# Kernel optimization log

Measured on AMD Instinct MI355X. Metric: run time of the kernel, lower is better.

The kernel has to match this reference:

```python
import jax, jax.numpy as jnp
import numpy as np
import math

H = 8        # num_heads
D = 1024     # per-head dim (d_q = d_k = d_v)
D_I = 1024   # image embed dim
D_L = 768    # sentence embed dim
EPS = 1e-5   # nn.LayerNorm default


def setup_inputs() -> dict:
    key = jax.random.key(0)
    ks = jax.random.split(key, 8)
    B, NQ, NK = 8, 196, 128
    img_embed = jax.random.normal(ks[0], (B, NQ, D_I), dtype=jnp.float32)
    sent_embed = jax.random.normal(ks[1], (B, NK, D_L), dtype=jnp.float32)
    atten_mask = jnp.ones((B, NK), dtype=jnp.int32)
    # weights stored [in, out] (equivalent to torch Linear weight.T), no bias
    Wq = jax.random.normal(ks[2], (D_I, H * D), dtype=jnp.float32) * (1.0 / math.sqrt(D_I))
    Wk = jax.random.normal(ks[3], (D_L, H * D), dtype=jnp.float32) * (1.0 / math.sqrt(D_L))
    Wv = jax.random.normal(ks[4], (D_L, H * D), dtype=jnp.float32) * (1.0 / math.sqrt(D_L))
    Wo = jax.random.normal(ks[5], (H * D, D_I), dtype=jnp.float32) * (1.0 / math.sqrt(H * D))
    gamma = jnp.ones((D_I,), dtype=jnp.float32)
    beta = jnp.zeros((D_I,), dtype=jnp.float32)
    return {"img_embed": img_embed, "sent_embed": sent_embed, "atten_mask": atten_mask,
            "Wq": Wq, "Wk": Wk, "Wv": Wv, "Wo": Wo, "gamma": gamma, "beta": beta}


def reference(img_embed, sent_embed, atten_mask, Wq, Wk, Wv, Wo, gamma, beta):
    B = img_embed.shape[0]
    # projections -> [B, N, H, D] -> [B, H, N, D]
    Q = (img_embed @ Wq).reshape(B, -1, H, D).transpose(0, 2, 1, 3)
    K = (sent_embed @ Wk).reshape(B, -1, H, D).transpose(0, 2, 1, 3)
    V = (sent_embed @ Wv).reshape(B, -1, H, D).transpose(0, 2, 1, 3)
    # scaled dot-product scores [B, H, NQ, NK]
    score = jnp.einsum('bhqd,bhkd->bhqk', Q, K) / math.sqrt(D)
    mask = (atten_mask != 0)[:, None, None, :]  # [B,1,1,NK]
    score = jnp.where(mask, score, -jnp.inf)
    attn = jax.nn.softmax(score, axis=-1)
    # PV -> [B, NQ, H, D] -> [B, NQ, H*D]
    ctx = jnp.einsum('bhqk,bhkd->bqhd', attn, V).reshape(B, -1, H * D)
    out = ctx @ Wo + img_embed  # residual
    # LayerNorm over last dim
    mu = jnp.mean(out, axis=-1, keepdims=True)
    var = jnp.var(out, axis=-1, keepdims=True)
    return (out - mu) * jax.lax.rsqrt(var + EPS) * gamma + beta
```

## Files before the change

### kernel.cpp

```cpp
#include <hip/hip_runtime.h>
#include <hip/hip_bf16.h>

#define BB 8
#define NQ 196
#define NKK 128
#define HH 8
#define DH 1024
#define DI 1024
#define DL 768
#define HD 8192
#define KSPLIT 8

typedef __attribute__((ext_vector_type(8))) short short8;
typedef __attribute__((ext_vector_type(4))) float f32x4;

__device__ inline unsigned short f2bf(float f) {
  unsigned int x = __float_as_uint(f);
  unsigned int r = (x + 0x7fffu + ((x >> 16) & 1u)) >> 16;
  return (unsigned short)r;
}

__device__ inline void gload16(const unsigned short* g, unsigned short* l) {
  __builtin_amdgcn_global_load_lds(
      (const __attribute__((address_space(1))) void*)g,
      (__attribute__((address_space(3))) void*)l, 16, 0, 0);
}

__global__ __launch_bounds__(256) void k_prep(
    const float* __restrict__ Wq, const float* __restrict__ Wk,
    const float* __restrict__ Wv, const float* __restrict__ Wo,
    const float* __restrict__ img, const float* __restrict__ sent,
    unsigned short* __restrict__ WqT, unsigned short* __restrict__ WkvT,
    unsigned short* __restrict__ WoT,
    unsigned short* __restrict__ imgB, unsigned short* __restrict__ sentB) {
  int b = blockIdx.x, t = threadIdx.x;
  if (b >= 7168) {
    const float* in; unsigned short* out; int i;
    if (b < 7952) { in = img;  out = imgB;  i = ((b - 7168) * 256 + t) * 8; }
    else          { in = sent; out = sentB; i = ((b - 7952) * 256 + t) * 8; }
    float4 x = *reinterpret_cast<const float4*>(in + i);
    float4 y = *reinterpret_cast<const float4*>(in + i + 4);
    short8 v;
    v[0] = (short)f2bf(x.x); v[1] = (short)f2bf(x.y);
    v[2] = (short)f2bf(x.z); v[3] = (short)f2bf(x.w);
    v[4] = (short)f2bf(y.x); v[5] = (short)f2bf(y.y);
    v[6] = (short)f2bf(y.z); v[7] = (short)f2bf(y.w);
    *reinterpret_cast<short8*>(out + i) = v;
    return;
  }
  const float* in; unsigned short* out; int R, C, bx;
  if (b < 2048)      { in = Wq; out = WqT;  R = DI; C = HD; bx = b; }
  else if (b < 3584) { in = Wk; out = WkvT; R = DL; C = HD; bx = b - 2048; }
  else if (b < 5120) { in = Wv; out = WkvT + (size_t)HD * DL; R = DL; C = HD; bx = b - 3584; }
  else               { in = Wo; out = WoT;  R = HD; C = DI; bx = b - 5120; }
  int nxc = C >> 6;
  int c0 = (bx % nxc) << 6, r0 = (bx / nxc) << 6;
  __shared__ float tile[64][65];
#pragma unroll
  for (int p = 0; p < 4; ++p) {
    int row = p * 16 + (t >> 4), c4 = (t & 15) << 2;
    float4 v = *reinterpret_cast<const float4*>(&in[(size_t)(r0 + row) * C + c0 + c4]);
    tile[row][c4] = v.x; tile[row][c4 + 1] = v.y;
    tile[row][c4 + 2] = v.z; tile[row][c4 + 3] = v.w;
  }
  __syncthreads();
#pragma unroll
  for (int p = 0; p < 2; ++p) {
    int cc = p * 32 + (t >> 3), r8 = (t & 7) << 3;
    short8 w;
#pragma unroll
    for (int j = 0; j < 8; ++j) w[j] = (short)f2bf(tile[r8 + j][cc]);
    *reinterpret_cast<short8*>(&out[(size_t)(c0 + cc) * R + r0 + r8]) = w;
  }
}

__global__ __launch_bounds__(256) void k_transpose_v(
    const unsigned short* __restrict__ Vp, unsigned short* __restrict__ Vt, int ld_in) {
  __shared__ unsigned short tile[32][34];
  int z = blockIdx.z, b = z >> 3, h = z & 7;
  const unsigned short* in = Vp + (size_t)b * NKK * ld_in + (size_t)h * DH;
  unsigned short* out = Vt + (size_t)z * DH * NKK;
  int d0 = blockIdx.x * 32, k0 = blockIdx.y * 32;
  {
    int rr = threadIdx.x >> 3, c4 = (threadIdx.x & 7) << 2;
    ushort4 v = *reinterpret_cast<const ushort4*>(&in[(size_t)(k0 + rr) * ld_in + d0 + c4]);
    tile[rr][c4] = v.x; tile[rr][c4 + 1] = v.y;
    tile[rr][c4 + 2] = v.z; tile[rr][c4 + 3] = v.w;
  }
  __syncthreads();
  {
    int cc = threadIdx.x >> 3, r4 = (threadIdx.x & 7) << 2;
    ushort4 w;
    w.x = tile[r4][cc];     w.y = tile[r4 + 1][cc];
    w.z = tile[r4 + 2][cc]; w.w = tile[r4 + 3][cc];
    *reinterpret_cast<ushort4*>(&out[(size_t)(d0 + cc) * NKK + k0 + r4]) = w;
  }
}


__device__ __attribute__((always_inline)) inline void ph_pre() {
  __builtin_amdgcn_s_barrier();
  asm volatile("s_waitcnt lgkmcnt(0)" ::: "memory");
  __builtin_amdgcn_sched_barrier(0);
  __builtin_amdgcn_s_setprio(1);
}
__device__ __attribute__((always_inline)) inline void ph_post() {
  __builtin_amdgcn_s_setprio(0);
  __builtin_amdgcn_s_barrier();
}
__device__ __attribute__((always_inline)) inline void ph_post_vm4() {
  __builtin_amdgcn_s_setprio(0);
  asm volatile("s_waitcnt vmcnt(4)" ::: "memory");
  __builtin_amdgcn_s_barrier();
}
__device__ __attribute__((always_inline)) inline void ph_post_vm0() {
  __builtin_amdgcn_s_setprio(0);
  asm volatile("s_waitcnt vmcnt(0)" ::: "memory");
  __builtin_amdgcn_s_barrier();
}

#define LDA8(d, buf, s)                                                          \
  { _Pragma("unroll") for (int mi = 0; mi < 4; ++mi) {                           \
      const int row_ = wm * 128 + (s) * 64 + mi * 16 + fr;                       \
      d[mi][0] = *reinterpret_cast<const short8*>(&As[buf][row_ * 64 + swz0]);   \
      d[mi][1] = *reinterpret_cast<const short8*>(&As[buf][row_ * 64 + swz1]);   \
    } }
#define LDB8(d, buf, s)                                                          \
  { _Pragma("unroll") for (int ni = 0; ni < 2; ++ni) {                           \
      const int row_ = wn * 64 + (s) * 32 + ni * 16 + fr;                        \
      d[ni][0] = *reinterpret_cast<const short8*>(&Bs[buf][row_ * 64 + swz0]);   \
      d[ni][1] = *reinterpret_cast<const short8*>(&Bs[buf][row_ * 64 + swz1]);   \
    } }
#define MMQ(a, sa, b, sb)                                                        \
  { _Pragma("unroll") for (int kk = 0; kk < 2; ++kk) {                           \
      _Pragma("unroll") for (int mi = 0; mi < 4; ++mi) {                         \
        _Pragma("unroll") for (int ni = 0; ni < 2; ++ni)                         \
          acc[(sa) * 4 + mi][(sb) * 2 + ni] =                                    \
              __builtin_amdgcn_mfma_f32_16x16x32_bf16(                           \
                  a[mi][kk], b[ni][kk], acc[(sa) * 4 + mi][(sb) * 2 + ni], 0, 0, 0); \
      } } }
#define STA8(buf, h, kof)                                                        \
  { gload16(aS[h][0] + (kof), &As[buf][(h) * 8192 + wid * 512]);                 \
    gload16(aS[h][1] + (kof), &As[buf][(h) * 8192 + 4096 + wid * 512]); }
#define STB8(buf, h, kof)                                                        \
  { gload16(bS[h][0] + (kof), &Bs[buf][(h) * 8192 + wid * 512]);                 \
    gload16(bS[h][1] + (kof), &Bs[buf][(h) * 8192 + 4096 + wid * 512]); }

struct GCfg {
  const unsigned short* A; const unsigned short* B; void* C;
  int M, K, lda, ldb, ldc, nx, ny;
  long aKC, bKC, cKC;
};

template<bool C_BF16>
__global__ __launch_bounds__(512, 2) void k_gemm8(GCfg c0, GCfg c1, int split) {
  __shared__ unsigned short As[2][16384];
  __shared__ unsigned short Bs[2][16384];

  const int seg = (int)blockIdx.x >= split;
  const GCfg cfg = seg ? c1 : c0;
  const int o = (int)blockIdx.x - (seg ? split : 0);
  const int nseg = seg ? ((int)gridDim.x - split) : split;
  const int qq = nseg >> 3;
  const int g = (o & 7) * qq + (o >> 3);
  const int ybl = g % cfg.ny; int t1 = g / cfg.ny;
  const int xbl = t1 % cfg.nx; const int kc = t1 / cfg.nx;

  const int M = cfg.M, lda = cfg.lda, ldb = cfg.ldb;
  const unsigned short* Ab = cfg.A + (size_t)kc * cfg.aKC;
  const unsigned short* Bb = cfg.B + (size_t)kc * cfg.bKC;

  const int tid = threadIdx.x, lane = tid & 63, wid = tid >> 6;
  const int wm = wid >> 2, wn = wid & 3;
  const int m_base = ybl * 256, n_base = xbl * 256;
  const int fr = lane & 15, qk = lane >> 4;
  const int swz0 = ((qk ^ (fr & 7)) << 3);
  const int swz1 = (((4 + qk) ^ (fr & 7)) << 3);

  const int srow = lane >> 3;
  const int sc8 = (((lane & 7) ^ srow) << 3);
  const unsigned short* aS[2][2];
  const unsigned short* bS[2][2];
#pragma unroll
  for (int h = 0; h < 2; ++h)
#pragma unroll
    for (int j = 0; j < 2; ++j) {
      int rm = m_base + h * 128 + j * 64 + wid * 8 + srow;
      rm = rm < M ? rm : M - 1;
      aS[h][j] = Ab + (size_t)rm * lda + sc8;
      bS[h][j] = Bb + (size_t)(n_base + h * 128 + j * 64 + wid * 8 + srow) * ldb + sc8;
    }

  short8 a0[4][2], a1[4][2], b0[2][2], b1[2][2];
  f32x4 acc[8][4] = {};

  const int NT = cfg.K >> 6;
  const int NIT = NT >> 1;

  STB8(0, 0, 0) STB8(0, 1, 0) STA8(0, 0, 0) STA8(0, 1, 0)
  STB8(1, 0, 64) STB8(1, 1, 64)
  asm volatile("s_waitcnt vmcnt(4)" ::: "memory");
  __builtin_amdgcn_s_barrier();

  for (int it = 0; it < NIT - 1; ++it) {
    const int t1k = (2 * it + 1) << 6;
    const int t2k = (2 * it + 2) << 6;
    const int t3k = (2 * it + 3) << 6;
    LDA8(a0, 0, 0) LDB8(b0, 0, 0) STA8(1, 0, t1k)
    ph_pre(); MMQ(a0, 0, b0, 0) ph_post();
    LDB8(b1, 0, 1) STA8(1, 1, t1k)
    ph_pre(); MMQ(a0, 0, b1, 1) ph_post();
    LDA8(a1, 0, 1) STB8(0, 0, t2k)
    ph_pre(); MMQ(a1, 1, b1, 1) ph_post();
    STB8(0, 1, t2k)
    ph_pre(); MMQ(a1, 1, b0, 0) ph_post_vm4();
    LDA8(a0, 1, 0) LDB8(b0, 1, 0) STA8(0, 0, t2k)
    ph_pre(); MMQ(a0, 0, b0, 0) ph_post();
    LDB8(b1, 1, 1) STA8(0, 1, t2k)
    ph_pre(); MMQ(a0, 0, b1, 1) ph_post();
    LDA8(a1, 1, 1) STB8(1, 0, t3k)
    ph_pre(); MMQ(a1, 1, b1, 1) ph_post();
    STB8(1, 1, t3k)
    ph_pre(); MMQ(a1, 1, b0, 0) ph_post_vm4();
  }

  {
    const int tlk = (NT - 1) << 6;
    LDA8(a0, 0, 0) LDB8(b0, 0, 0) STA8(1, 0, tlk)
    ph_pre(); MMQ(a0, 0, b0, 0) ph_post();
    LDB8(b1, 0, 1) STA8(1, 1, tlk)
    ph_pre(); MMQ(a0, 0, b1, 1) ph_post();
    LDA8(a1, 0, 1)
    ph_pre(); MMQ(a1, 1, b1, 1) ph_post();
    ph_pre(); MMQ(a1, 1, b0, 0) ph_post_vm0();
    LDA8(a0, 1, 0) LDB8(b0, 1, 0)
    ph_pre(); MMQ(a0, 0, b0, 0) ph_post();
    LDB8(b1, 1, 1)
    ph_pre(); MMQ(a0, 0, b1, 1) ph_post();
    LDA8(a1, 1, 1)
    ph_pre(); MMQ(a1, 1, b1, 1) ph_post();
    ph_pre(); MMQ(a1, 1, b0, 0)
    __builtin_amdgcn_s_setprio(0);
  }

  const size_t cOff = (size_t)kc * cfg.cKC;
  const int ldc = cfg.ldc;
  const int rq4 = qk * 4;
#pragma unroll
  for (int mi = 0; mi < 8; ++mi) {
#pragma unroll
    for (int ni = 0; ni < 4; ++ni) {
      int col = n_base + wn * 64 + ni * 16 + fr;
#pragma unroll
      for (int i = 0; i < 4; ++i) {
        int row = m_base + wm * 128 + mi * 16 + rq4 + i;
        if (row < M) {
          float val = acc[mi][ni][i];
          size_t off = cOff + (size_t)row * ldc + col;
          if constexpr (C_BF16) ((unsigned short*)cfg.C)[off] = f2bf(val);
          else                  ((float*)cfg.C)[off] = val;
        }
      }
    }
  }
}

template<bool C_BF16>
__global__ __launch_bounds__(256, 2) void k_gemm3(
    const unsigned short* __restrict__ A, const unsigned short* __restrict__ B,
    void* __restrict__ Cptr,
    int M, int K, int lda, int ldb, int ldc,
    int nx, int ny, int ZBH,
    long aSB, long aSH, long bSB, long bSH, long cSB, long cSH,
    long aKC, long bKC, long cKC) {
  __shared__ unsigned short As[8192];
  __shared__ unsigned short Bs[8192];

  const int nblk = gridDim.x;
  const int qq = nblk >> 3, rr = nblk & 7;
  int g;
  { const int o = blockIdx.x, xcd = o & 7, i = o >> 3;
    g = (xcd < rr ? xcd * (qq + 1) : rr * (qq + 1) + (xcd - rr) * qq) + i; }
  const int ybl = g % ny; int t1 = g / ny;
  const int xbl = t1 % nx; const int zz = t1 / nx;
  const int kc = zz / ZBH, bh = zz % ZBH;
  const int zb = bh >> 3, zh = bh & 7;

  const unsigned short* Ab = A + (size_t)zb * aSB + (size_t)zh * aSH + (size_t)kc * aKC;
  const unsigned short* Bb = B + (size_t)zb * bSB + (size_t)zh * bSH + (size_t)kc * bKC;

  const int tid = threadIdx.x, lane = tid & 63, wid = tid >> 6;
  const int wm = wid >> 1, wn = wid & 1;
  const int m_base = ybl * 128, n_base = xbl * 128;

  const int r0 = wid * 32 + (lane >> 3);
  const int sc8 = (((lane & 7) ^ (lane >> 3)) << 3);
  const unsigned short* aSrc[4];
  const unsigned short* bSrc[4];
#pragma unroll
  for (int p = 0; p < 4; ++p) {
    int rm = m_base + r0 + p * 8; rm = rm < M ? rm : M - 1;
    aSrc[p] = Ab + (size_t)rm * lda + sc8;
    bSrc[p] = Bb + (size_t)(n_base + r0 + p * 8) * ldb + sc8;
  }

  const int fr = lane & 15;
  const int qk = lane >> 4;
  f32x4 acc[4][4] = {};

  for (int k0 = 0; k0 < K; k0 += 64) {
#pragma unroll
    for (int p = 0; p < 4; ++p) gload16(aSrc[p] + k0, &As[wid * 2048 + p * 512]);
#pragma unroll
    for (int p = 0; p < 4; ++p) gload16(bSrc[p] + k0, &Bs[wid * 2048 + p * 512]);
    __syncthreads();
#pragma unroll
    for (int kk = 0; kk < 2; ++kk) {
      short8 af[4], bfr[4];
#pragma unroll
      for (int mi = 0; mi < 4; ++mi) {
        int row = wm * 64 + mi * 16 + fr;
        int swz = ((kk * 4 + qk) ^ (row & 7)) << 3;
        af[mi] = *reinterpret_cast<const short8*>(&As[row * 64 + swz]);
      }
#pragma unroll
      for (int ni = 0; ni < 4; ++ni) {
        int row = wn * 64 + ni * 16 + fr;
        int swz = ((kk * 4 + qk) ^ (row & 7)) << 3;
        bfr[ni] = *reinterpret_cast<const short8*>(&Bs[row * 64 + swz]);
      }
#pragma unroll
      for (int mi = 0; mi < 4; ++mi)
#pragma unroll
        for (int ni = 0; ni < 4; ++ni)
          acc[mi][ni] = __builtin_amdgcn_mfma_f32_16x16x32_bf16(af[mi], bfr[ni], acc[mi][ni], 0, 0, 0);
    }
    __syncthreads();
  }

  const size_t cOff = (size_t)zb * cSB + (size_t)zh * cSH + (size_t)kc * cKC;
  const int rq = qk * 4;
#pragma unroll
  for (int mi = 0; mi < 4; ++mi) {
#pragma unroll
    for (int ni = 0; ni < 4; ++ni) {
      int col = n_base + wn * 64 + ni * 16 + fr;
#pragma unroll
      for (int i = 0; i < 4; ++i) {
        int row = m_base + wm * 64 + mi * 16 + rq + i;
        if (row < M) {
          float val = acc[mi][ni][i];
          size_t off = cOff + (size_t)row * ldc + col;
          if constexpr (C_BF16) ((unsigned short*)Cptr)[off] = f2bf(val);
          else                  ((float*)Cptr)[off] = val;
        }
      }
    }
  }
}

#define S_PART ((size_t)64 * NQ * NKK)
__global__ __launch_bounds__(256) void k_softmax(
    const float* __restrict__ S, unsigned short* __restrict__ P, const int* __restrict__ mask) {
  int row = blockIdx.x * 4 + (threadIdx.x >> 6);
  if (row >= BB * HH * NQ) return;
  int lane = threadIdx.x & 63;
  int b = row / (HH * NQ);
  const float* s = S + (size_t)row * NKK;
  float s0 = (s[lane]      + s[lane + S_PART])      * 0.03125f;
  float s1 = (s[lane + 64] + s[lane + 64 + S_PART]) * 0.03125f;
  const int* mrow = mask + b * NKK;
  if (mrow[lane] == 0)      s0 = -1e30f;
  if (mrow[lane + 64] == 0) s1 = -1e30f;
  float mx = fmaxf(s0, s1);
#pragma unroll
  for (int d = 32; d; d >>= 1) mx = fmaxf(mx, __shfl_xor(mx, d));
  float e0 = __expf(s0 - mx), e1 = __expf(s1 - mx);
  float sum = e0 + e1;
#pragma unroll
  for (int d = 32; d; d >>= 1) sum += __shfl_xor(sum, d);
  float inv = 1.0f / sum;
  P[(size_t)row * NKK + lane]      = f2bf(e0 * inv);
  P[(size_t)row * NKK + lane + 64] = f2bf(e1 * inv);
}

__global__ __launch_bounds__(256) void k_layernorm_red(
    const float* __restrict__ Parts, const float* __restrict__ resid,
    const float* __restrict__ gamma, const float* __restrict__ beta,
    float* __restrict__ out, int M) {
  int row = blockIdx.x;
  int tid = threadIdx.x;
  const size_t stride = (size_t)M * DI;
  const float* p = Parts + (size_t)row * DI;
  const float* r = resid + (size_t)row * DI;
  float v[4], sum = 0.f, sq = 0.f;
#pragma unroll
  for (int i = 0; i < 4; ++i) {
    int c = tid + i * 256;
    float acc = r[c];
#pragma unroll
    for (int k = 0; k < KSPLIT; ++k) acc += p[k * stride + c];
    v[i] = acc; sum += acc; sq += acc * acc;
  }
#pragma unroll
  for (int d = 32; d; d >>= 1) { sum += __shfl_xor(sum, d); sq += __shfl_xor(sq, d); }
  __shared__ float ssum[4], ssq[4];
  int w = tid >> 6;
  if ((tid & 63) == 0) { ssum[w] = sum; ssq[w] = sq; }
  __syncthreads();
  sum = ssum[0] + ssum[1] + ssum[2] + ssum[3];
  sq  = ssq[0]  + ssq[1]  + ssq[2]  + ssq[3];
  float mean = sum * (1.0f / DI);
  float var  = sq * (1.0f / DI) - mean * mean;
  float rstd = rsqrtf(var + 1e-5f);
  float* o = out + (size_t)row * DI;
#pragma unroll
  for (int i = 0; i < 4; ++i) {
    int c = tid + i * 256;
    o[c] = (v[i] - mean) * rstd * gamma[c] + beta[c];
  }
}

extern "C" void kernel_launch(void* const* d_in, const int* in_sizes, int n_in,
                              void* d_out, int out_size, void* d_ws, size_t ws_size,
                              hipStream_t stream) {
  const float* img   = (const float*)d_in[0];
  const float* sent  = (const float*)d_in[1];
  const int*   mask  = (const int*)d_in[2];
  const float* Wq    = (const float*)d_in[3];
  const float* Wk    = (const float*)d_in[4];
  const float* Wv    = (const float*)d_in[5];
  const float* Wo    = (const float*)d_in[6];
  const float* gamma = (const float*)d_in[7];
  const float* beta  = (const float*)d_in[8];
  float* out = (float*)d_out;

  char* ws = (char*)d_ws;
  unsigned short* WoT   = (unsigned short*)(ws);
  unsigned short* WkvT  = (unsigned short*)(ws + 16777216);
  unsigned short* Vt    = (unsigned short*)(ws + 16777216);
  float*          Oac   = (float*)         (ws + 16777216);
  float*          S2    = (float*)         (ws + 33554432);
  unsigned short* P     = (unsigned short*)(ws + 46399488);
  unsigned short* Qb    = (unsigned short*)(ws + 49610752);
  unsigned short* KVb   = (unsigned short*)(ws + 75300864);
  unsigned short* ctx   = (unsigned short*)(ws + 75300864);
  unsigned short* WqT   = (unsigned short*)(ws + 75300864);
  unsigned short* imgB  = (unsigned short*)(ws + 92078080);
  unsigned short* sentB = (unsigned short*)(ws + 108855296);

  dim3 tb(256);
  dim3 tb8(512);

  k_prep<<<dim3(8336), tb, 0, stream>>>(Wq, Wk, Wv, Wo, img, sent,
                                        WqT, WkvT, WoT, imgB, sentB);

  GCfg cfgQ  = { imgB,  WqT,  Qb,  BB * NQ,  DI, DI, DI, HD,      32, 7, 0, 0, 0 };
  GCfg cfgKV = { sentB, WkvT, KVb, BB * NKK, DL, DL, DL, 2 * HD,  64, 4, 0, 0, 0 };
  k_gemm8<true><<<dim3(224 + 256), tb8, 0, stream>>>(cfgQ, cfgKV, 224);

  k_transpose_v<<<dim3(DH / 32, NKK / 32, BB * HH), tb, 0, stream>>>(KVb + HD, Vt, 2 * HD);

  k_gemm3<false><<<dim3(2 * 1 * 128), tb, 0, stream>>>(
      Qb, KVb, S2, NQ, DH / 2, HD, 2 * HD, NKK,
      1, 2, 64,
      (long)NQ * HD, (long)DH, (long)NKK * 2 * HD, (long)DH,
      (long)HH * NQ * NKK, (long)NQ * NKK,
      (long)(DH / 2), (long)(DH / 2), (long)64 * NQ * NKK);

  k_softmax<<<dim3(BB * HH * NQ / 4), tb, 0, stream>>>(S2, P, mask);

  k_gemm3<true><<<dim3(2 * 8 * 64), tb, 0, stream>>>(
      P, Vt, ctx, NQ, NKK, NKK, NKK, HD,
      8, 2, 64,
      (long)HH * NQ * NKK, (long)NQ * NKK, (long)HH * DH * NKK, (long)DH * NKK,
      (long)NQ * HD, (long)DH, 0, 0, 0);

  GCfg cfgO = { ctx, WoT, Oac, BB * NQ, HD / KSPLIT, HD, HD, DI, 4, 7,
                (long)(HD / KSPLIT), (long)(HD / KSPLIT), (long)(BB * NQ) * DI };
  k_gemm8<false><<<dim3(224), tb8, 0, stream>>>(cfgO, cfgO, 224);

  k_layernorm_red<<<dim3(BB * NQ), tb, 0, stream>>>(Oac, img, gamma, beta, out, BB * NQ);
}
```

Before: 187.5 us.

## Store Q/K/V, context and Wo in head-blocked 1024-wide chunks

The projection GEMM epilogue now writes Q, K and V head-blocked, each head's 1024 columns stored as a contiguous chunk with row stride 1024 instead of interleaved rows of 8192 or 16384. The Wo transpose, the V transpose, the attention GEMMs and the output GEMM are re-strided to match. Per-head and per-K-split tiles therefore become dense 2 KB-stride regions, which is meant to improve locality and reduce TLB and cache-set pressure. It adds some index arithmetic in the epilogues, and every stride in the chain has to stay consistent.

Result: no change. 187.1 us (-0.2%).

```diff
diff --git a/kernel.cpp b/kernel.cpp
--- a/kernel.cpp
+++ b/kernel.cpp
@@ -10,6 +10,9 @@
 #define DL 768
 #define HD 8192
 #define KSPLIT 8
+#define MTOT (BB * NQ)
+#define CHK (MTOT * DH)
+#define KVCHK (1024 * 1024)
 
 typedef __attribute__((ext_vector_type(8))) short short8;
 typedef __attribute__((ext_vector_type(4))) float f32x4;
@@ -48,11 +51,11 @@
     *reinterpret_cast<short8*>(out + i) = v;
     return;
   }
-  const float* in; unsigned short* out; int R, C, bx;
+  const float* in; unsigned short* out; int R, C, bx; bool kcb = false;
   if (b < 2048)      { in = Wq; out = WqT;  R = DI; C = HD; bx = b; }
   else if (b < 3584) { in = Wk; out = WkvT; R = DL; C = HD; bx = b - 2048; }
   else if (b < 5120) { in = Wv; out = WkvT + (size_t)HD * DL; R = DL; C = HD; bx = b - 3584; }
-  else               { in = Wo; out = WoT;  R = HD; C = DI; bx = b - 5120; }
+  else               { in = Wo; out = WoT;  R = HD; C = DI; bx = b - 5120; kcb = true; }
   int nxc = C >> 6;
   int c0 = (bx % nxc) << 6, r0 = (bx / nxc) << 6;
   __shared__ float tile[64][65];
@@ -70,20 +73,25 @@
     short8 w;
 #pragma unroll
     for (int j = 0; j < 8; ++j) w[j] = (short)f2bf(tile[r8 + j][cc]);
-    *reinterpret_cast<short8*>(&out[(size_t)(c0 + cc) * R + r0 + r8]) = w;
+    size_t off;
+    if (kcb)
+      off = ((size_t)(r0 >> 10) << 20) + (size_t)(c0 + cc) * 1024 + (r0 & 1023) + r8;
+    else
+      off = (size_t)(c0 + cc) * R + r0 + r8;
+    *reinterpret_cast<short8*>(&out[off]) = w;
   }
 }
 
 __global__ __launch_bounds__(256) void k_transpose_v(
-    const unsigned short* __restrict__ Vp, unsigned short* __restrict__ Vt, int ld_in) {
+    const unsigned short* __restrict__ Vbase, unsigned short* __restrict__ Vt) {
   __shared__ unsigned short tile[32][34];
   int z = blockIdx.z, b = z >> 3, h = z & 7;
-  const unsigned short* in = Vp + (size_t)b * NKK * ld_in + (size_t)h * DH;
+  const unsigned short* in = Vbase + ((size_t)h << 20) + (size_t)b * NKK * 1024;
   unsigned short* out = Vt + (size_t)z * DH * NKK;
   int d0 = blockIdx.x * 32, k0 = blockIdx.y * 32;
   {
     int rr = threadIdx.x >> 3, c4 = (threadIdx.x & 7) << 2;
-    ushort4 v = *reinterpret_cast<const ushort4*>(&in[(size_t)(k0 + rr) * ld_in + d0 + c4]);
+    ushort4 v = *reinterpret_cast<const ushort4*>(&in[(size_t)(k0 + rr) * 1024 + d0 + c4]);
     tile[rr][c4] = v.x; tile[rr][c4 + 1] = v.y;
     tile[rr][c4 + 2] = v.z; tile[rr][c4 + 3] = v.w;
   }
@@ -152,7 +160,7 @@
   long aKC, bKC, cKC;
 };
 
-template<bool C_BF16>
+template<bool C_BF16, bool HB>
 __global__ __launch_bounds__(512, 2) void k_gemm8(GCfg c0, GCfg c1, int split) {
   __shared__ unsigned short As[2][16384];
   __shared__ unsigned short Bs[2][16384];
@@ -256,7 +264,11 @@
         int row = m_base + wm * 128 + mi * 16 + rq4 + i;
         if (row < M) {
           float val = acc[mi][ni][i];
-          size_t off = cOff + (size_t)row * ldc + col;
+          size_t off;
+          if constexpr (HB)
+            off = (size_t)(col >> 10) * cfg.cKC + (size_t)row * ldc + (col & 1023);
+          else
+            off = cOff + (size_t)row * ldc + col;
           if constexpr (C_BF16) ((unsigned short*)cfg.C)[off] = f2bf(val);
           else                  ((float*)cfg.C)[off] = val;
         }
@@ -455,30 +467,34 @@
   k_prep<<<dim3(8336), tb, 0, stream>>>(Wq, Wk, Wv, Wo, img, sent,
                                         WqT, WkvT, WoT, imgB, sentB);
 
-  GCfg cfgQ  = { imgB,  WqT,  Qb,  BB * NQ,  DI, DI, DI, HD,      32, 7, 0, 0, 0 };
-  GCfg cfgKV = { sentB, WkvT, KVb, BB * NKK, DL, DL, DL, 2 * HD,  64, 4, 0, 0, 0 };
-  k_gemm8<true><<<dim3(224 + 256), tb8, 0, stream>>>(cfgQ, cfgKV, 224);
-
-  k_transpose_v<<<dim3(DH / 32, NKK / 32, BB * HH), tb, 0, stream>>>(KVb + HD, Vt, 2 * HD);
+  GCfg cfgQ  = { imgB,  WqT,  Qb,  MTOT,     DI, DI, DI, 1024, 32, 7, 0, 0, (long)CHK };
+  GCfg cfgKV = { sentB, WkvT, KVb, BB * NKK, DL, DL, DL, 1024, 64, 4, 0, 0, (long)KVCHK };
+  k_gemm8<true, true><<<dim3(224 + 256), tb8, 0, stream>>>(cfgQ, cfgKV, 224);
+
+  k_transpose_v<<<dim3(DH / 32, NKK / 32, BB * HH), tb, 0, stream>>>(
+      KVb + ((size_t)8 << 20), Vt);
 
   k_gemm3<false><<<dim3(2 * 1 * 128), tb, 0, stream>>>(
-      Qb, KVb, S2, NQ, DH / 2, HD, 2 * HD, NKK,
+      Qb, KVb, S2, NQ, DH / 2, 1024, 1024, NKK,
       1, 2, 64,
-      (long)NQ * HD, (long)DH, (long)NKK * 2 * HD, (long)DH,
+      (long)NQ * 1024, (long)CHK,
+      (long)NKK * 1024, (long)KVCHK,
       (long)HH * NQ * NKK, (long)NQ * NKK,
       (long)(DH / 2), (long)(DH / 2), (long)64 * NQ * NKK);
 
   k_softmax<<<dim3(BB * HH * NQ / 4), tb, 0, stream>>>(S2, P, mask);
 
   k_gemm3<true><<<dim3(2 * 8 * 64), tb, 0, stream>>>(
-      P, Vt, ctx, NQ, NKK, NKK, NKK, HD,
+      P, Vt, ctx, NQ, NKK, NKK, NKK, 1024,
       8, 2, 64,
-      (long)HH * NQ * NKK, (long)NQ * NKK, (long)HH * DH * NKK, (long)DH * NKK,
-      (long)NQ * HD, (long)DH, 0, 0, 0);
-
-  GCfg cfgO = { ctx, WoT, Oac, BB * NQ, HD / KSPLIT, HD, HD, DI, 4, 7,
-                (long)(HD / KSPLIT), (long)(HD / KSPLIT), (long)(BB * NQ) * DI };
-  k_gemm8<false><<<dim3(224), tb8, 0, stream>>>(cfgO, cfgO, 224);
+      (long)HH * NQ * NKK, (long)NQ * NKK,
+      (long)HH * DH * NKK, (long)DH * NKK,
+      (long)NQ * 1024, (long)CHK,
+      0, 0, 0);
+
+  GCfg cfgO = { ctx, WoT, Oac, MTOT, HD / KSPLIT, 1024, 1024, DI, 4, 7,
+                (long)CHK, (long)KVCHK, (long)CHK };
+  k_gemm8<false, false><<<dim3(224), tb8, 0, stream>>>(cfgO, cfgO, 224);
 
   k_layernorm_red<<<dim3(BB * NQ), tb, 0, stream>>>(Oac, img, gamma, beta, out, BB * NQ);
 }
```
